# Kernel optimization log

Hardware: AMD Instinct MI355X
Metric: run time of the kernel (lower is better)

The kernel has to match this reference:

```python
import jax, jax.numpy as jnp
import numpy as np

B, K, D, V = 4096, 128, 512, 128000


def setup_inputs() -> dict:
    key = jax.random.key(0)
    k1, k2, k3 = jax.random.split(key, 3)
    inp = jax.random.normal(k1, (B, D), dtype=jnp.float32)
    indices = jax.random.randint(k2, (B, K), 0, V, dtype=jnp.int64)
    # xavier_uniform: bound = sqrt(6/(fan_in+fan_out)) for weight [V, D]
    bound = float(np.sqrt(6.0 / (V + D)))
    weight = jax.random.uniform(k3, (V, D), dtype=jnp.float32, minval=-bound, maxval=bound)
    bias = jnp.zeros((V,), dtype=jnp.float32)
    return {"inp": inp, "indices": indices, "sparse": 1, "weight": weight, "bias": bias}


def reference(inp, indices, sparse, weight, bias):
    if sparse:
        # gather per-sample weight rows [B, K, D] and bias [B, K], then batched dot
        w = weight[indices]          # [B, K, D]
        b = bias[indices]            # [B, K]
        out = jnp.einsum('bkd,bd->bk', w, inp) + b
        return out
    else:
        return inp @ weight.T + bias
```

## Files before the change

### kernel.cpp

```cpp
#include <hip/hip_runtime.h>


constexpr int Kc = 128;
constexpr int Dc = 512;

__global__ __launch_bounds__(256) void SparseProjection_kernel(
    const float* __restrict__ inp,
    const int*   __restrict__ indices,
    const float* __restrict__ weight,
    const float* __restrict__ bias,
    float*       __restrict__ out)
{
    const int b    = blockIdx.x;
    const int tid  = threadIdx.x;
    const int lane = tid & 63;
    const int wave = tid >> 6;

    const float4* inp_row = (const float4*)(inp + (size_t)b * Dc);
    const float4 a0 = inp_row[lane];
    const float4 a1 = inp_row[64 + lane];

    const int* idx_base  = indices + (size_t)b * Kc;
    float*     out_base  = out     + (size_t)b * Kc;

    #pragma unroll 4
    for (int i = 0; i < 32; ++i) {
        const int k   = wave * 32 + i;
        const int idx = idx_base[k];
        const float4* wrow = (const float4*)(weight + (size_t)idx * Dc);

        const float4 w0 = wrow[lane];
        const float4 w1 = wrow[64 + lane];

        float s = a0.x * w0.x + a0.y * w0.y + a0.z * w0.z + a0.w * w0.w
                + a1.x * w1.x + a1.y * w1.y + a1.z * w1.z + a1.w * w1.w;

        #pragma unroll
        for (int off = 32; off > 0; off >>= 1)
            s += __shfl_xor(s, off, 64);

        if (lane == 0)
            out_base[k] = s + bias[idx];
    }
}

extern "C" void kernel_launch(void* const* d_in, const int* in_sizes, int n_in,
                              void* d_out, int out_size, void* d_ws, size_t ws_size,
                              hipStream_t stream) {
    const float* inp     = (const float*)d_in[0];
    const int*   indices = (const int*)  d_in[1];
    const float* weight  = (const float*)d_in[3];
    const float* bias    = (const float*)d_in[4];
    float*       out     = (float*)d_out;

    const int B = in_sizes[0] / Dc;
    SparseProjection_kernel<<<B, 256, 0, stream>>>(inp, indices, weight, bias, out);
}
```

Measured before the change: 448.8 us.

## Counting-sort indices by vocab row so each weight row is read once

Replaces the per-sample gather with a counting sort of (sample, k) pairs by vocabulary index. The sort is built from a histogram, a three-pass prefix scan and an atomic scatter into workspace. A new compute kernel assigns one wave per weight row, loads that row once, and dots it against every input row that references it, writing scattered outputs. This is meant to cut repeated random weight-row traffic down to a single pass over the weight matrix. In exchange it adds six extra launches plus a memset, and atomic contention. Input rows are now re-read randomly, and output writes are scattered 4-byte stores.

```diff
diff --git a/kernel.cpp b/kernel.cpp
--- a/kernel.cpp
+++ b/kernel.cpp
@@ -1,8 +1,10 @@
 #include <hip/hip_runtime.h>
+#include <stdint.h>
 
 
 constexpr int Kc = 128;
 constexpr int Dc = 512;
+constexpr int Vc = 128000;
 
 __global__ __launch_bounds__(256) void SparseProjection_kernel(
     const float* __restrict__ inp,
@@ -41,6 +43,132 @@
 
         if (lane == 0)
             out_base[k] = s + bias[idx];
+    }
+}
+
+
+__global__ __launch_bounds__(256) void hist_kernel(
+    const int* __restrict__ idx, unsigned int* __restrict__ counts, int n)
+{
+    int i      = blockIdx.x * blockDim.x + threadIdx.x;
+    int stride = gridDim.x * blockDim.x;
+    for (; i < n; i += stride)
+        atomicAdd(&counts[idx[i]], 1u);
+}
+
+__global__ __launch_bounds__(256) void scan1_kernel(
+    const unsigned int* __restrict__ counts, unsigned int* __restrict__ partials)
+{
+    __shared__ unsigned int sm[256];
+    const int c = blockIdx.x;
+    const int t = threadIdx.x;
+    unsigned int a = counts[c * 512 + 2 * t] + counts[c * 512 + 2 * t + 1];
+    sm[t] = a;
+    __syncthreads();
+    for (int off = 128; off > 0; off >>= 1) {
+        if (t < off) sm[t] += sm[t + off];
+        __syncthreads();
+    }
+    if (t == 0) partials[c] = sm[0];
+}
+
+__global__ __launch_bounds__(256) void scan2_kernel(
+    unsigned int* __restrict__ partials, int nch)
+{
+    __shared__ unsigned int sm[256];
+    const int t = threadIdx.x;
+    unsigned int v = (t < nch) ? partials[t] : 0u;
+    sm[t] = v;
+    __syncthreads();
+    for (int off = 1; off < 256; off <<= 1) {
+        unsigned int add = (t >= off) ? sm[t - off] : 0u;
+        __syncthreads();
+        sm[t] += add;
+        __syncthreads();
+    }
+    if (t < nch) partials[t] = sm[t] - v;
+}
+
+__global__ __launch_bounds__(256) void scan3_kernel(
+    unsigned int* __restrict__ counts,
+    const unsigned int* __restrict__ partials,
+    unsigned int* __restrict__ starts,
+    int n_total)
+{
+    __shared__ unsigned int sm[256];
+    const int c    = blockIdx.x;
+    const int t    = threadIdx.x;
+    const int base = c * 512;
+    unsigned int c0 = counts[base + 2 * t];
+    unsigned int c1 = counts[base + 2 * t + 1];
+    unsigned int pair = c0 + c1;
+    sm[t] = pair;
+    __syncthreads();
+    for (int off = 1; off < 256; off <<= 1) {
+        unsigned int add = (t >= off) ? sm[t - off] : 0u;
+        __syncthreads();
+        sm[t] += add;
+        __syncthreads();
+    }
+    unsigned int excl = sm[t] - pair + partials[c];
+    unsigned int s0 = excl;
+    unsigned int s1 = excl + c0;
+    starts[base + 2 * t]     = s0;
+    starts[base + 2 * t + 1] = s1;
+    counts[base + 2 * t]     = s0;
+    counts[base + 2 * t + 1] = s1;
+    if (c == 0 && t == 0) starts[Vc] = (unsigned int)n_total;
+}
+
+__global__ __launch_bounds__(256) void scatter_kernel(
+    const int* __restrict__ idx, unsigned int* __restrict__ cursor,
+    unsigned int* __restrict__ sorted, int n)
+{
+    int i      = blockIdx.x * blockDim.x + threadIdx.x;
+    int stride = gridDim.x * blockDim.x;
+    for (; i < n; i += stride) {
+        int v = idx[i];
+        unsigned int pos = atomicAdd(&cursor[v], 1u);
+        sorted[pos] = (unsigned int)i;
+    }
+}
+
+__global__ __launch_bounds__(256) void compute_sorted_kernel(
+    const float* __restrict__ inp,
+    const float* __restrict__ weight,
+    const float* __restrict__ bias,
+    const unsigned int* __restrict__ starts,
+    const unsigned int* __restrict__ sorted,
+    float* __restrict__ out)
+{
+    const int lane = threadIdx.x & 63;
+    const int wave = threadIdx.x >> 6;
+    const int v    = blockIdx.x * 4 + wave;
+
+    const unsigned int s = starts[v];
+    const unsigned int e = starts[v + 1];
+    if (s == e) return;
+
+    const float4* wrow = (const float4*)(weight + (size_t)v * Dc);
+    const float4 w0 = wrow[lane];
+    const float4 w1 = wrow[64 + lane];
+    const float  bv = bias[v];
+
+    for (unsigned int j = s; j < e; ++j) {
+        const unsigned int bk = sorted[j];
+        const float4* arow = (const float4*)(inp + (size_t)(bk >> 7) * Dc);
+        const float4 a0 = arow[lane];
+        const float4 a1 = arow[64 + lane];
+
+        float sdot = a0.x * w0.x + a0.y * w0.y + a0.z * w0.z + a0.w * w0.w
+                   + a1.x * w1.x + a1.y * w1.y + a1.z * w1.z + a1.w * w1.w;
+
+        #pragma unroll
+        for (int off = 32; off > 0; off >>= 1)
+            sdot += __shfl_xor(sdot, off, 64);
+
+        if (lane == 0)
+            out[bk] = sdot + bv;
     }
 }
 
@@ -54,5 +182,27 @@
     float*       out     = (float*)d_out;
 
     const int B = in_sizes[0] / Dc;
-    SparseProjection_kernel<<<B, 256, 0, stream>>>(inp, indices, weight, bias, out);
-}
+    const int n = B * Kc;
+
+    const size_t need_u32 = (size_t)2 * Vc + 64 + (size_t)n + 256;
+    if (ws_size < need_u32 * sizeof(unsigned int)) {
+        SparseProjection_kernel<<<B, 256, 0, stream>>>(inp, indices, weight, bias, out);
+        return;
+    }
+
+    unsigned int* ws       = (unsigned int*)d_ws;
+    unsigned int* counts   = ws;
+    unsigned int* starts   = ws + Vc;
+    unsigned int* sorted   = ws + 2 * Vc + 64;
+    unsigned int* partials = sorted + n;
+
+    hipMemsetAsync(counts, 0, (size_t)Vc * sizeof(unsigned int), stream);
+
+    hist_kernel<<<2048, 256, 0, stream>>>(indices, counts, n);
+    scan1_kernel<<<Vc / 512, 256, 0, stream>>>(counts, partials);
+    scan2_kernel<<<1, 256, 0, stream>>>(partials, Vc / 512);
+    scan3_kernel<<<Vc / 512, 256, 0, stream>>>(counts, partials, starts, n);
+    scatter_kernel<<<2048, 256, 0, stream>>>(indices, counts, sorted, n);
+
+    compute_sorted_kernel<<<Vc / 4, 256, 0, stream>>>(inp, weight, bias, starts, sorted, out);
+}
```

New measurement: 472.9 us. +5.4%, slower.

## Assign one weight row per half-wave and preload indices via lane shuffles

Applied to the files above, without the earlier changes.

Each 32-lane half-wave now computes one output element per iteration, so every wave works on two gathered weight rows at once. Each lane loads four float4 vectors instead of two, and the cross-lane reduction drops to five shuffles. The 16 row indices for each half-wave are loaded once up front and broadcast with __shfl, replacing a per-iteration index load. The grid is also split into two launches over halves of the batch, which adds a second launch's overhead and gives each lane a strided 64-byte access pattern per row.

```diff
diff --git a/kernel.cpp b/kernel.cpp
--- a/kernel.cpp
+++ b/kernel.cpp
@@ -4,43 +4,58 @@
 constexpr int Kc = 128;
 constexpr int Dc = 512;
 
+typedef float f4 __attribute__((ext_vector_type(4)));
+
+__device__ __forceinline__ float dot4(f4 a, f4 w) {
+    return a.x * w.x + a.y * w.y + a.z * w.z + a.w * w.w;
+}
+
 __global__ __launch_bounds__(256) void SparseProjection_kernel(
     const float* __restrict__ inp,
     const int*   __restrict__ indices,
     const float* __restrict__ weight,
     const float* __restrict__ bias,
-    float*       __restrict__ out)
+    float*       __restrict__ out,
+    int bOff)
 {
-    const int b    = blockIdx.x;
+    const int b    = bOff + blockIdx.x;
     const int tid  = threadIdx.x;
     const int lane = tid & 63;
-    const int wave = tid >> 6;
+    const int l32  = lane & 31;
+    const int h    = (lane >> 5);
+    const int hw   = tid >> 5;
 
-    const float4* inp_row = (const float4*)(inp + (size_t)b * Dc);
-    const float4 a0 = inp_row[lane];
-    const float4 a1 = inp_row[64 + lane];
+    const f4* ir = (const f4*)(inp + (size_t)b * Dc);
+    const f4 a0 = ir[4 * l32 + 0];
+    const f4 a1 = ir[4 * l32 + 1];
+    const f4 a2 = ir[4 * l32 + 2];
+    const f4 a3 = ir[4 * l32 + 3];
 
-    const int* idx_base  = indices + (size_t)b * Kc;
-    float*     out_base  = out     + (size_t)b * Kc;
+    const int* idx_base = indices + (size_t)b * Kc + hw * 16;
+    const int  s_idx    = idx_base[lane & 15];
+
+    float* out_base = out + (size_t)b * Kc + hw * 16;
 
     #pragma unroll 4
-    for (int i = 0; i < 32; ++i) {
-        const int k   = wave * 32 + i;
-        const int idx = idx_base[k];
-        const float4* wrow = (const float4*)(weight + (size_t)idx * Dc);
+    for (int it = 0; it < 16; ++it) {
+        const int idx = __shfl(s_idx, h * 32 + it, 64);
 
-        const float4 w0 = wrow[lane];
-        const float4 w1 = wrow[64 + lane];
+        const f4* wr = (const f4*)(weight + (size_t)idx * Dc);
+        const f4 w0 = wr[4 * l32 + 0];
+        const f4 w1 = wr[4 * l32 + 1];
+        const f4 w2 = wr[4 * l32 + 2];
+        const f4 w3 = wr[4 * l32 + 3];
 
-        float s = a0.x * w0.x + a0.y * w0.y + a0.z * w0.z + a0.w * w0.w
-                + a1.x * w1.x + a1.y * w1.y + a1.z * w1.z + a1.w * w1.w;
+        float s = dot4(a0, w0) + dot4(a1, w1) + dot4(a2, w2) + dot4(a3, w3);
 
-        #pragma unroll
-        for (int off = 32; off > 0; off >>= 1)
-            s += __shfl_xor(s, off, 64);
+        s += __shfl_xor(s, 16, 64);
+        s += __shfl_xor(s,  8, 64);
+        s += __shfl_xor(s,  4, 64);
+        s += __shfl_xor(s,  2, 64);
+        s += __shfl_xor(s,  1, 64);
 
-        if (lane == 0)
-            out_base[k] = s + bias[idx];
+        if (l32 == 0)
+            out_base[it] = s + bias[idx];
     }
 }
 
@@ -54,5 +69,12 @@
     float*       out     = (float*)d_out;
 
     const int B = in_sizes[0] / Dc;
-    SparseProjection_kernel<<<B, 256, 0, stream>>>(inp, indices, weight, bias, out);
+
+    if ((B & 1) == 0) {
+        const int Bh = B / 2;
+        SparseProjection_kernel<<<Bh, 256, 0, stream>>>(inp, indices, weight, bias, out, 0);
+        SparseProjection_kernel<<<Bh, 256, 0, stream>>>(inp, indices, weight, bias, out, Bh);
+    } else {
+        SparseProjection_kernel<<<B, 256, 0, stream>>>(inp, indices, weight, bias, out, 0);
+    }
 }
```

Result: no change. 454.2 us (+1.2%).
